# Kernel tuning notes

Measured on AMD Instinct MI355X. Metric: run time of the kernel, lower is better.

## Reference

```python
import jax, jax.numpy as jnp
import numpy as np

jax.config.update("jax_enable_x64", True)  # 64-bit hashes for collision-free WL signatures

N_NODES = 100_000
N_FEATURES = 64
N_EDGES = 6_400_000
NUM_ITERATIONS = 3
STEP = 1


def setup_inputs() -> dict:
    key = jax.random.key(0)
    kx, ke = jax.random.split(key)
    x = jax.random.normal(kx, (N_NODES, N_FEATURES), dtype=jnp.float32)  # one-hot-ish label scores
    edge_index = jax.random.randint(ke, (2, N_EDGES), 0, N_NODES, dtype=jnp.int64)
    return {"x": x, "edge_index": edge_index}


def _splitmix64(z):
    # High-quality 64-bit mixer (uint64, wraps mod 2^64).
    z = z + jnp.uint64(0x9E3779B97F4A7C15)
    z = (z ^ (z >> jnp.uint64(30))) * jnp.uint64(0xBF58476D1CE4E5B9)
    z = (z ^ (z >> jnp.uint64(27))) * jnp.uint64(0x94D049BB133111EB)
    return z ^ (z >> jnp.uint64(31))


def _wl_conv(colors, src, dst, offset):
    """One WL refinement: hash (own color, multiset of neighbor colors), then
    relabel signatures by first-occurrence order (matches PyG WLConv's dict
    insertion order), continuing the global color counter `offset` (matches the
    persistent hashmap across iterations)."""
    n = colors.shape[0]
    h = _splitmix64(colors.astype(jnp.uint64) + jnp.uint64(1))
    # multiset of neighbor colors -> order-invariant sum of neighbor hashes
    nb_sum = jnp.zeros(n, dtype=jnp.uint64).at[dst].add(h[src])  # [N]
    sig = _splitmix64(h * jnp.uint64(0x100000001B3) + nb_sum)    # [N] signatures
    # first-occurrence relabeling (stable, deterministic)
    _, inv = jnp.unique(sig, size=n, fill_value=jnp.uint64(0), return_inverse=True)
    idx = jnp.arange(n, dtype=jnp.int64)
    first_idx = jax.ops.segment_min(idx, inv, num_segments=n)  # empty segments -> int64 max
    order = jnp.argsort(first_idx)                              # real uniques come first
    ranks = jnp.zeros(n, dtype=jnp.int64).at[order].set(idx)
    new_colors = offset + ranks[inv]
    num_new = jnp.sum(first_idx < n).astype(jnp.int64)
    return new_colors, offset + num_new


def reference(x, edge_index):
    src, dst = edge_index[0], edge_index[1]
    colors = jnp.argmax(x, axis=1).astype(jnp.int64)  # [N]
    feats = [colors]
    offset = jnp.int64(0)
    for _ in range(NUM_ITERATIONS):
        for _ in range(STEP):
            colors, offset = _wl_conv(colors, src, dst, offset)
        feats.append(colors)
    return jnp.stack(feats, axis=-1)  # [N, NUM_ITERATIONS+1], int64
```

## Files before the change

### kernel.cpp

```cpp
#include <hip/hip_runtime.h>

typedef unsigned long long u64;
typedef unsigned int u32;

#define TBL_BITS 18
#define TBL_SIZE (1u << TBL_BITS)
#define TBL_MASK (TBL_SIZE - 1u)
#define EMPTY_KEY 0xFFFFFFFFFFFFFFFFull

#define NB   196
#define NBLK 128
#define CNT_ENTRIES (NB * NBLK)

__device__ __forceinline__ u64 splitmix64(u64 z) {
    z = z + 0x9E3779B97F4A7C15ull;
    z = (z ^ (z >> 30)) * 0xBF58476D1CE4E5B9ull;
    z = (z ^ (z >> 27)) * 0x94D049BB133111EBull;
    return z ^ (z >> 31);
}


__global__ void argmax_kernel(const float* __restrict__ x, u64* __restrict__ h,
                              int* __restrict__ out, u32* __restrict__ offsets, int n) {
    if (blockIdx.x == 0 && threadIdx.x == 0) offsets[0] = 0u;
    int wave = (int)((blockIdx.x * (u32)blockDim.x + threadIdx.x) >> 6);
    int lane = threadIdx.x & 63;
    if (wave >= n) return;
    float v = x[(size_t)wave * 64 + lane];
    int idx = lane;
    #pragma unroll
    for (int off = 32; off >= 1; off >>= 1) {
        float ov = __shfl_xor(v, off);
        int   oi = __shfl_xor(idx, off);
        if (ov > v || (ov == v && oi < idx)) { v = ov; idx = oi; }
    }
    if (lane == 0) {
        h[wave] = splitmix64((u64)idx + 1ull);
        out[(size_t)wave * 4 + 0] = idx;
    }
}

__global__ void sig_kernel(const u64* __restrict__ h, const u64* __restrict__ nb,
                           u64* __restrict__ sig, u64* __restrict__ keys,
                           u32* __restrict__ vals, int n) {
    int i = blockIdx.x * blockDim.x + threadIdx.x;
    if (i >= n) return;
    u64 s = splitmix64(h[i] * 0x100000001B3ull + nb[i]);
    sig[i] = s;
    u32 slot = (u32)s & TBL_MASK;
    while (true) {
        u64 prev = atomicCAS(&keys[slot], (u64)EMPTY_KEY, s);
        if (prev == EMPTY_KEY || prev == s) break;
        slot = (slot + 1u) & TBL_MASK;
    }
    atomicMin(&vals[slot], (u32)i);
}


__global__ __launch_bounds__(1024) void count_part(const int* __restrict__ dst,
                                                   u32* __restrict__ cnt, int m) {
    __shared__ u32 hist[NB];
    int t = threadIdx.x, b = blockIdx.x;
    if (t < NB) hist[t] = 0u;
    __syncthreads();
    int per = (m + NBLK - 1) / NBLK;
    int lo = b * per, hi = lo + per; if (hi > m) hi = m;
    for (int e = lo + t; e < hi; e += 1024) atomicAdd(&hist[((u32)dst[e]) >> 9], 1u);
    __syncthreads();
    if (t < NB) cnt[t * NBLK + b] = hist[t];
}

__global__ __launch_bounds__(1024) void scan_flat(const u32* __restrict__ cnt,
                                                  u32* __restrict__ off) {
    __shared__ u32 A[1024], B[1024];
    int t = threadIdx.x;
    int chunk = (CNT_ENTRIES + 1023) / 1024;
    int lo = t * chunk, hi = lo + chunk;
    if (lo > CNT_ENTRIES) lo = CNT_ENTRIES;
    if (hi > CNT_ENTRIES) hi = CNT_ENTRIES;
    u32 s = 0;
    for (int i = lo; i < hi; ++i) s += cnt[i];
    A[t] = s; __syncthreads();
    u32 *cur = A, *nxt = B;
    for (int o = 1; o < 1024; o <<= 1) {
        u32 v = cur[t] + ((t >= o) ? cur[t - o] : 0u);
        nxt[t] = v; __syncthreads();
        u32* tmp = cur; cur = nxt; nxt = tmp;
    }
    u32 run = cur[t] - s;
    for (int i = lo; i < hi; ++i) { off[i] = run; run += cnt[i]; }
}

__global__ __launch_bounds__(1024) void scatter_part(const int* __restrict__ src,
                                                     const int* __restrict__ dst,
                                                     const u32* __restrict__ off,
                                                     u32* __restrict__ packed, int m) {
    __shared__ u32 pos[NB];
    int t = threadIdx.x, b = blockIdx.x;
    if (t < NB) pos[t] = off[t * NBLK + b];
    __syncthreads();
    int per = (m + NBLK - 1) / NBLK;
    int lo = b * per, hi = lo + per; if (hi > m) hi = m;
    for (int e = lo + t; e < hi; e += 1024) {
        u32 d = (u32)dst[e];
        u32 p = atomicAdd(&pos[d >> 9], 1u);
        packed[p] = ((u32)src[e] << 9) | (d & 511u);
    }
}

__global__ __launch_bounds__(1024) void nb_kernel(const u32* __restrict__ packed,
                                                  const u32* __restrict__ off,
                                                  const u64* __restrict__ h,
                                                  u64* __restrict__ nb,
                                                  u64* __restrict__ keys,
                                                  u32* __restrict__ vals, int n, int m) {
    int b = blockIdx.x, t = threadIdx.x;
    if (b >= NB) {
        int j = (b - NB) * 1024 + t;
        keys[j] = EMPTY_KEY; vals[j] = 0xFFFFFFFFu;
        return;
    }
    __shared__ u64 acc[512];
    if (t < 512) acc[t] = 0ull;
    __syncthreads();
    int lo = (int)off[b * NBLK];
    int hi = (b == NB - 1) ? m : (int)off[(b + 1) * NBLK];
    for (int e = lo + t; e < hi; e += 1024) {
        u32 p = packed[e];
        atomicAdd(&acc[p & 511u], h[p >> 9]);
    }
    __syncthreads();
    int base = b * 512;
    if (t < 512 && base + t < n) nb[base + t] = acc[t];
}

__global__ void count_rank(const u64* __restrict__ sig, const u64* __restrict__ keys,
                           const u32* __restrict__ vals, u32* __restrict__ f,
                           u32* __restrict__ lrank, u32* __restrict__ partials, int n) {
    int b = blockIdx.x, t = threadIdx.x;
    int i = b * 256 + t;
    u32 isf = 0, fi = 0;
    if (i < n) {
        u64 s = sig[i];
        u32 slot = (u32)s & TBL_MASK;
        while (keys[slot] != s) slot = (slot + 1u) & TBL_MASK;
        fi = vals[slot];
        f[i] = fi;
        isf = (fi == (u32)i) ? 1u : 0u;
    }
    __shared__ u32 wsum[4];
    u32 lane = t & 63, wv = (u32)t >> 6;
    int x = (int)isf;
    #pragma unroll
    for (int o = 1; o < 64; o <<= 1) {
        int y = __shfl_up(x, o);
        if (lane >= (u32)o) x += y;
    }
    if (lane == 63) wsum[wv] = (u32)x;
    __syncthreads();
    u32 woff = 0;
    for (u32 w = 0; w < wv; ++w) woff += wsum[w];
    if (i < n) lrank[i] = woff + (u32)x - isf;
    if (t == 255) partials[b] = woff + (u32)x;
}

__global__ void scan_partials(const u32* __restrict__ partials, u32* __restrict__ pp,
                              u32* __restrict__ offsets, int iter, int nblk) {
    __shared__ u32 A[512], B[512];
    int t = threadIdx.x;
    u32 v = (t < nblk) ? partials[t] : 0u;
    A[t] = v; __syncthreads();
    u32 *cur = A, *nxt = B;
    for (int o = 1; o < 512; o <<= 1) {
        u32 y = cur[t] + ((t >= o) ? cur[t - o] : 0u);
        nxt[t] = y; __syncthreads();
        u32* tmp = cur; cur = nxt; nxt = tmp;
    }
    if (t < nblk) pp[t] = cur[t] - v;
    if (t == 511) offsets[iter + 1] = offsets[iter] + cur[511];
}

__global__ void relabel_fast(const u32* __restrict__ f, const u32* __restrict__ lrank,
                             const u32* __restrict__ pp, const u32* __restrict__ offsets,
                             int iter, u64* __restrict__ h, int* __restrict__ out, int n) {
    int i = blockIdx.x * 256 + threadIdx.x;
    if (i >= n) return;
    u32 j = f[i];
    u32 c = offsets[iter] + pp[j >> 8] + lrank[j];
    h[i] = splitmix64((u64)c + 1ull);
    out[(size_t)i * 4 + (iter + 1)] = (int)c;
}


__global__ void init_iter_kernel(u64* __restrict__ keys, u32* __restrict__ vals,
                                 u64* __restrict__ nb, int n) {
    int i = blockIdx.x * blockDim.x + threadIdx.x;
    if (i < (int)TBL_SIZE) { keys[i] = EMPTY_KEY; vals[i] = 0xFFFFFFFFu; }
    if (i < n) nb[i] = 0ull;
}

__global__ void edge_kernel(const int* __restrict__ src, const int* __restrict__ dst,
                            const u64* __restrict__ h, u64* __restrict__ nb, int m) {
    int stride = gridDim.x * blockDim.x;
    for (int e = blockIdx.x * blockDim.x + threadIdx.x; e < m; e += stride) {
        atomicAdd(&nb[(u32)dst[e]], h[(u32)src[e]]);
    }
}

extern "C" void kernel_launch(void* const* d_in, const int* in_sizes, int n_in,
                              void* d_out, int out_size, void* d_ws, size_t ws_size,
                              hipStream_t stream) {
    const float* x = (const float*)d_in[0];
    const int* ei = (const int*)d_in[1];
    int n = in_sizes[0] / 64;
    int m = in_sizes[1] / 2;
    const int* src = ei;
    const int* dst = ei + m;
    int* out = (int*)d_out;

    const int NPB = (n + 255) / 256;

    auto align = [](size_t v) { return (v + 255) & ~(size_t)255; };
    size_t sz_packed = align((size_t)m * 4);
    size_t sz_cnt    = align((size_t)CNT_ENTRIES * 4);
    size_t sz_h      = align((size_t)n * 8);
    size_t sz_tblk   = align((size_t)TBL_SIZE * 8);
    size_t sz_tblv   = align((size_t)TBL_SIZE * 4);
    size_t sz_n4     = align((size_t)n * 4);
    size_t sz_small  = align((size_t)512 * 4);
    size_t need_fast = sz_packed + 2 * sz_cnt + 3 * sz_h + sz_tblk + sz_tblv
                     + 2 * sz_n4 + 2 * sz_small + 256;

    char* p = (char*)d_ws;
    if (ws_size >= need_fast) {
        u32* packed  = (u32*)p; p += sz_packed;
        u32* cnt     = (u32*)p; p += sz_cnt;
        u32* off     = (u32*)p; p += sz_cnt;
        u64* h       = (u64*)p; p += sz_h;
        u64* nb      = (u64*)p; p += sz_h;
        u64* sig     = (u64*)p; p += sz_h;
        u64* keys    = (u64*)p; p += sz_tblk;
        u32* vals    = (u32*)p; p += sz_tblv;
        u32* f       = (u32*)p; p += sz_n4;
        u32* lrank   = (u32*)p; p += sz_n4;
        u32* partials= (u32*)p; p += sz_small;
        u32* pp      = (u32*)p; p += sz_small;
        u32* offsets = (u32*)p;

        argmax_kernel<<<(n + 3) / 4, 256, 0, stream>>>(x, h, out, offsets, n);
        count_part  <<<NBLK, 1024, 0, stream>>>(dst, cnt, m);
        scan_flat   <<<1, 1024, 0, stream>>>(cnt, off);
        scatter_part<<<NBLK, 1024, 0, stream>>>(src, dst, off, packed, m);

        for (int it = 0; it < 3; ++it) {
            nb_kernel    <<<NB + 256, 1024, 0, stream>>>(packed, off, h, nb, keys, vals, n, m);
            sig_kernel   <<<NPB, 256, 0, stream>>>(h, nb, sig, keys, vals, n);
            count_rank   <<<NPB, 256, 0, stream>>>(sig, keys, vals, f, lrank, partials, n);
            scan_partials<<<1, 512, 0, stream>>>(partials, pp, offsets, it, NPB);
            relabel_fast <<<NPB, 256, 0, stream>>>(f, lrank, pp, offsets, it, h, out, n);
        }
    } else {
        u64* h       = (u64*)p; p += sz_h;
        u64* nb      = (u64*)p; p += sz_h;
        u64* sig     = (u64*)p; p += sz_h;
        u64* keys    = (u64*)p; p += sz_tblk;
        u32* vals    = (u32*)p; p += sz_tblv;
        u32* f       = (u32*)p; p += sz_n4;
        u32* lrank   = (u32*)p; p += sz_n4;
        u32* partials= (u32*)p; p += sz_small;
        u32* pp      = (u32*)p; p += sz_small;
        u32* offsets = (u32*)p;

        argmax_kernel<<<(n + 3) / 4, 256, 0, stream>>>(x, h, out, offsets, n);
        for (int it = 0; it < 3; ++it) {
            init_iter_kernel<<<(TBL_SIZE + 255) / 256, 256, 0, stream>>>(keys, vals, nb, n);
            edge_kernel  <<<4096, 256, 0, stream>>>(src, dst, h, nb, m);
            sig_kernel   <<<NPB, 256, 0, stream>>>(h, nb, sig, keys, vals, n);
            count_rank   <<<NPB, 256, 0, stream>>>(sig, keys, vals, f, lrank, partials, n);
            scan_partials<<<1, 512, 0, stream>>>(partials, pp, offsets, it, NPB);
            relabel_fast <<<NPB, 256, 0, stream>>>(f, lrank, pp, offsets, it, h, out, n);
        }
    }
}
```

Baseline: 308.1 us.

## Use finer destination buckets with vectorized partitioning and cached hash slots

The edge partition moves from 196 buckets of 512 nodes to 782 buckets of 128 nodes, using 256 partition blocks and int4/uint4 vectorized loads. A two-level scan with 64-aligned bucket bases replaces the single-thread-block flat scan. The neighbor-sum kernel now runs many more small blocks, each with a 128-entry shared accumulator, to raise parallelism and cut shared-memory atomic footprint per block. The signature kernel also stores the hash-table slot so count_rank skips the re-probe and no longer needs the sig array. In exchange, the fast path only runs when the edge count is a multiple of 4 and the bucket count fits in 1024.

```diff
diff --git a/kernel.cpp b/kernel.cpp
--- a/kernel.cpp
+++ b/kernel.cpp
@@ -8,9 +8,10 @@
 #define TBL_MASK (TBL_SIZE - 1u)
 #define EMPTY_KEY 0xFFFFFFFFFFFFFFFFull
 
-#define NB   196
-#define NBLK 128
-#define CNT_ENTRIES (NB * NBLK)
+#define BK_BITS 7
+#define BK_SZ   128
+#define MAXNB   1024
+#define NBLK    256
 
 __device__ __forceinline__ u64 splitmix64(u64 z) {
     z = z + 0x9E3779B97F4A7C15ull;
@@ -18,7 +19,6 @@
     z = (z ^ (z >> 27)) * 0x94D049BB133111EBull;
     return z ^ (z >> 31);
 }
-
 
 __global__ void argmax_kernel(const float* __restrict__ x, u64* __restrict__ h,
                               int* __restrict__ out, u32* __restrict__ offsets, int n) {
@@ -40,13 +40,145 @@
     }
 }
 
+
+__global__ __launch_bounds__(1024) void count_part(const int* __restrict__ dst,
+                                                   u32* __restrict__ cnt, int m, int nbuck) {
+    __shared__ u32 hist[MAXNB];
+    int t = threadIdx.x, b = blockIdx.x;
+    for (int i = t; i < nbuck; i += 1024) hist[i] = 0u;
+    __syncthreads();
+    int mv = m >> 2;
+    int perv = (mv + NBLK - 1) / NBLK;
+    int lo = b * perv, hi = lo + perv; if (hi > mv) hi = mv;
+    const int4* d4 = (const int4*)dst;
+    for (int i = lo + t; i < hi; i += 1024) {
+        int4 v = d4[i];
+        atomicAdd(&hist[((u32)v.x) >> BK_BITS], 1u);
+        atomicAdd(&hist[((u32)v.y) >> BK_BITS], 1u);
+        atomicAdd(&hist[((u32)v.z) >> BK_BITS], 1u);
+        atomicAdd(&hist[((u32)v.w) >> BK_BITS], 1u);
+    }
+    if (b == 0 && t == 0)
+        for (int e = mv * 4; e < m; ++e) atomicAdd(&hist[((u32)dst[e]) >> BK_BITS], 1u);
+    __syncthreads();
+    for (int i = t; i < nbuck; i += 1024) cnt[i * NBLK + b] = hist[i];
+}
+
+__global__ void scan_bucket(u32* __restrict__ cnt, u32* __restrict__ total, int nbuck) {
+    int b = blockIdx.x, t = threadIdx.x;
+    u32 v = cnt[b * NBLK + t];
+    int lane = t & 63, w = t >> 6;
+    int x = (int)v;
+    #pragma unroll
+    for (int o = 1; o < 64; o <<= 1) {
+        int y = __shfl_up(x, o);
+        if (lane >= o) x += y;
+    }
+    __shared__ u32 ws[4];
+    if (lane == 63) ws[w] = (u32)x;
+    __syncthreads();
+    u32 woff = 0;
+    for (int ww = 0; ww < w; ++ww) woff += ws[ww];
+    u32 incl = woff + (u32)x;
+    cnt[b * NBLK + t] = incl - v;
+    if (t == 255) total[b] = incl;
+}
+
+__global__ __launch_bounds__(1024) void scan_bases(const u32* __restrict__ total,
+                                                   u32* __restrict__ bases, int nbuck) {
+    __shared__ u32 A[1024], B[1024];
+    int t = threadIdx.x;
+    u32 pt = (t < nbuck) ? ((total[t] + 63u) & ~63u) : 0u;
+    A[t] = pt; __syncthreads();
+    u32 *cur = A, *nxt = B;
+    for (int o = 1; o < 1024; o <<= 1) {
+        u32 y = cur[t] + ((t >= o) ? cur[t - o] : 0u);
+        nxt[t] = y; __syncthreads();
+        u32* tmp = cur; cur = nxt; nxt = tmp;
+    }
+    if (t < nbuck) bases[t] = cur[t] - pt;
+}
+
+__global__ __launch_bounds__(1024) void scatter_part(const int* __restrict__ src,
+                                                     const int* __restrict__ dst,
+                                                     const u32* __restrict__ cnt,
+                                                     const u32* __restrict__ bases,
+                                                     u32* __restrict__ packed, int m, int nbuck) {
+    __shared__ u32 pos[MAXNB];
+    int t = threadIdx.x, b = blockIdx.x;
+    for (int i = t; i < nbuck; i += 1024) pos[i] = bases[i] + cnt[i * NBLK + b];
+    __syncthreads();
+    int mv = m >> 2;
+    int perv = (mv + NBLK - 1) / NBLK;
+    int lo = b * perv, hi = lo + perv; if (hi > mv) hi = mv;
+    const int4* d4 = (const int4*)dst;
+    const int4* s4 = (const int4*)src;
+    for (int i = lo + t; i < hi; i += 1024) {
+        int4 dv = d4[i]; int4 sv = s4[i];
+        u32 d0 = (u32)dv.x, d1 = (u32)dv.y, d2 = (u32)dv.z, d3 = (u32)dv.w;
+        u32 p0 = atomicAdd(&pos[d0 >> BK_BITS], 1u);
+        packed[p0] = ((u32)sv.x << BK_BITS) | (d0 & (BK_SZ - 1u));
+        u32 p1 = atomicAdd(&pos[d1 >> BK_BITS], 1u);
+        packed[p1] = ((u32)sv.y << BK_BITS) | (d1 & (BK_SZ - 1u));
+        u32 p2 = atomicAdd(&pos[d2 >> BK_BITS], 1u);
+        packed[p2] = ((u32)sv.z << BK_BITS) | (d2 & (BK_SZ - 1u));
+        u32 p3 = atomicAdd(&pos[d3 >> BK_BITS], 1u);
+        packed[p3] = ((u32)sv.w << BK_BITS) | (d3 & (BK_SZ - 1u));
+    }
+    if (b == 0 && t == 0) {
+        for (int e = mv * 4; e < m; ++e) {
+            u32 d = (u32)dst[e];
+            u32 p = atomicAdd(&pos[d >> BK_BITS], 1u);
+            packed[p] = ((u32)src[e] << BK_BITS) | (d & (BK_SZ - 1u));
+        }
+    }
+}
+
+__global__ __launch_bounds__(256) void nb_kernel(const u32* __restrict__ packed,
+                                                 const u32* __restrict__ bases,
+                                                 const u32* __restrict__ total,
+                                                 const u64* __restrict__ h,
+                                                 u64* __restrict__ nb,
+                                                 u64* __restrict__ keys,
+                                                 u32* __restrict__ vals, int n, int nbuck) {
+    int b = blockIdx.x, t = threadIdx.x;
+    if (b >= nbuck) {
+        int base = (b - nbuck) * 1024;
+        for (int k = t; k < 1024; k += 256) { keys[base + k] = EMPTY_KEY; vals[base + k] = 0xFFFFFFFFu; }
+        return;
+    }
+    __shared__ u64 acc[BK_SZ];
+    if (t < BK_SZ) acc[t] = 0ull;
+    __syncthreads();
+    u32 lo = bases[b];
+    u32 len = total[b];
+    const uint4* p4 = (const uint4*)(packed + lo);
+    int len4 = (int)(len >> 2);
+    for (int i = t; i < len4; i += 256) {
+        uint4 v = p4[i];
+        atomicAdd(&acc[v.x & (BK_SZ - 1u)], h[v.x >> BK_BITS]);
+        atomicAdd(&acc[v.y & (BK_SZ - 1u)], h[v.y >> BK_BITS]);
+        atomicAdd(&acc[v.z & (BK_SZ - 1u)], h[v.z >> BK_BITS]);
+        atomicAdd(&acc[v.w & (BK_SZ - 1u)], h[v.w >> BK_BITS]);
+    }
+    for (int e = len4 * 4 + t; e < (int)len; e += 256) {
+        u32 v = packed[lo + e];
+        atomicAdd(&acc[v & (BK_SZ - 1u)], h[v >> BK_BITS]);
+    }
+    __syncthreads();
+    if (t < BK_SZ) {
+        int node = (b << BK_BITS) + t;
+        if (node < n) nb[node] = acc[t];
+    }
+}
+
+
 __global__ void sig_kernel(const u64* __restrict__ h, const u64* __restrict__ nb,
-                           u64* __restrict__ sig, u64* __restrict__ keys,
+                           u32* __restrict__ slotarr, u64* __restrict__ keys,
                            u32* __restrict__ vals, int n) {
     int i = blockIdx.x * blockDim.x + threadIdx.x;
     if (i >= n) return;
     u64 s = splitmix64(h[i] * 0x100000001B3ull + nb[i]);
-    sig[i] = s;
     u32 slot = (u32)s & TBL_MASK;
     while (true) {
         u64 prev = atomicCAS(&keys[slot], (u64)EMPTY_KEY, s);
@@ -54,97 +186,17 @@
         slot = (slot + 1u) & TBL_MASK;
     }
     atomicMin(&vals[slot], (u32)i);
-}
-
-
-__global__ __launch_bounds__(1024) void count_part(const int* __restrict__ dst,
-                                                   u32* __restrict__ cnt, int m) {
-    __shared__ u32 hist[NB];
-    int t = threadIdx.x, b = blockIdx.x;
-    if (t < NB) hist[t] = 0u;
-    __syncthreads();
-    int per = (m + NBLK - 1) / NBLK;
-    int lo = b * per, hi = lo + per; if (hi > m) hi = m;
-    for (int e = lo + t; e < hi; e += 1024) atomicAdd(&hist[((u32)dst[e]) >> 9], 1u);
-    __syncthreads();
-    if (t < NB) cnt[t * NBLK + b] = hist[t];
-}
-
-__global__ __launch_bounds__(1024) void scan_flat(const u32* __restrict__ cnt,
-                                                  u32* __restrict__ off) {
-    __shared__ u32 A[1024], B[1024];
-    int t = threadIdx.x;
-    int chunk = (CNT_ENTRIES + 1023) / 1024;
-    int lo = t * chunk, hi = lo + chunk;
-    if (lo > CNT_ENTRIES) lo = CNT_ENTRIES;
-    if (hi > CNT_ENTRIES) hi = CNT_ENTRIES;
-    u32 s = 0;
-    for (int i = lo; i < hi; ++i) s += cnt[i];
-    A[t] = s; __syncthreads();
-    u32 *cur = A, *nxt = B;
-    for (int o = 1; o < 1024; o <<= 1) {
-        u32 v = cur[t] + ((t >= o) ? cur[t - o] : 0u);
-        nxt[t] = v; __syncthreads();
-        u32* tmp = cur; cur = nxt; nxt = tmp;
-    }
-    u32 run = cur[t] - s;
-    for (int i = lo; i < hi; ++i) { off[i] = run; run += cnt[i]; }
-}
-
-__global__ __launch_bounds__(1024) void scatter_part(const int* __restrict__ src,
-                                                     const int* __restrict__ dst,
-                                                     const u32* __restrict__ off,
-                                                     u32* __restrict__ packed, int m) {
-    __shared__ u32 pos[NB];
-    int t = threadIdx.x, b = blockIdx.x;
-    if (t < NB) pos[t] = off[t * NBLK + b];
-    __syncthreads();
-    int per = (m + NBLK - 1) / NBLK;
-    int lo = b * per, hi = lo + per; if (hi > m) hi = m;
-    for (int e = lo + t; e < hi; e += 1024) {
-        u32 d = (u32)dst[e];
-        u32 p = atomicAdd(&pos[d >> 9], 1u);
-        packed[p] = ((u32)src[e] << 9) | (d & 511u);
-    }
-}
-
-__global__ __launch_bounds__(1024) void nb_kernel(const u32* __restrict__ packed,
-                                                  const u32* __restrict__ off,
-                                                  const u64* __restrict__ h,
-                                                  u64* __restrict__ nb,
-                                                  u64* __restrict__ keys,
-                                                  u32* __restrict__ vals, int n, int m) {
-    int b = blockIdx.x, t = threadIdx.x;
-    if (b >= NB) {
-        int j = (b - NB) * 1024 + t;
-        keys[j] = EMPTY_KEY; vals[j] = 0xFFFFFFFFu;
-        return;
-    }
-    __shared__ u64 acc[512];
-    if (t < 512) acc[t] = 0ull;
-    __syncthreads();
-    int lo = (int)off[b * NBLK];
-    int hi = (b == NB - 1) ? m : (int)off[(b + 1) * NBLK];
-    for (int e = lo + t; e < hi; e += 1024) {
-        u32 p = packed[e];
-        atomicAdd(&acc[p & 511u], h[p >> 9]);
-    }
-    __syncthreads();
-    int base = b * 512;
-    if (t < 512 && base + t < n) nb[base + t] = acc[t];
-}
-
-__global__ void count_rank(const u64* __restrict__ sig, const u64* __restrict__ keys,
-                           const u32* __restrict__ vals, u32* __restrict__ f,
-                           u32* __restrict__ lrank, u32* __restrict__ partials, int n) {
+    slotarr[i] = slot;
+}
+
+__global__ void count_rank(const u32* __restrict__ slotarr, const u32* __restrict__ vals,
+                           u32* __restrict__ f, u32* __restrict__ lrank,
+                           u32* __restrict__ partials, int n) {
     int b = blockIdx.x, t = threadIdx.x;
     int i = b * 256 + t;
     u32 isf = 0, fi = 0;
     if (i < n) {
-        u64 s = sig[i];
-        u32 slot = (u32)s & TBL_MASK;
-        while (keys[slot] != s) slot = (slot + 1u) & TBL_MASK;
-        fi = vals[slot];
+        fi = vals[slotarr[i]];
         f[i] = fi;
         isf = (fi == (u32)i) ? 1u : 0u;
     }
@@ -219,28 +271,32 @@
     int* out = (int*)d_out;
 
     const int NPB = (n + 255) / 256;
+    const int nbuck = (n + BK_SZ - 1) >> BK_BITS;
 
     auto align = [](size_t v) { return (v + 255) & ~(size_t)255; };
-    size_t sz_packed = align((size_t)m * 4);
-    size_t sz_cnt    = align((size_t)CNT_ENTRIES * 4);
+    size_t sz_packed = align((size_t)m * 4 + (size_t)MAXNB * 64 * 4);
+    size_t sz_cnt    = align((size_t)MAXNB * NBLK * 4);
+    size_t sz_bt     = align((size_t)MAXNB * 4);
     size_t sz_h      = align((size_t)n * 8);
     size_t sz_tblk   = align((size_t)TBL_SIZE * 8);
     size_t sz_tblv   = align((size_t)TBL_SIZE * 4);
     size_t sz_n4     = align((size_t)n * 4);
     size_t sz_small  = align((size_t)512 * 4);
-    size_t need_fast = sz_packed + 2 * sz_cnt + 3 * sz_h + sz_tblk + sz_tblv
-                     + 2 * sz_n4 + 2 * sz_small + 256;
+    size_t need_fast = sz_packed + sz_cnt + 2 * sz_bt + 2 * sz_h + sz_tblk + sz_tblv
+                     + 3 * sz_n4 + 2 * sz_small + 256;
 
     char* p = (char*)d_ws;
-    if (ws_size >= need_fast) {
+    bool fast = (ws_size >= need_fast) && (nbuck <= MAXNB) && ((m & 3) == 0) && (NPB <= 512);
+    if (fast) {
         u32* packed  = (u32*)p; p += sz_packed;
         u32* cnt     = (u32*)p; p += sz_cnt;
-        u32* off     = (u32*)p; p += sz_cnt;
+        u32* total   = (u32*)p; p += sz_bt;
+        u32* bases   = (u32*)p; p += sz_bt;
         u64* h       = (u64*)p; p += sz_h;
         u64* nb      = (u64*)p; p += sz_h;
-        u64* sig     = (u64*)p; p += sz_h;
         u64* keys    = (u64*)p; p += sz_tblk;
         u32* vals    = (u32*)p; p += sz_tblv;
+        u32* slotarr = (u32*)p; p += sz_n4;
         u32* f       = (u32*)p; p += sz_n4;
         u32* lrank   = (u32*)p; p += sz_n4;
         u32* partials= (u32*)p; p += sz_small;
@@ -248,23 +304,24 @@
         u32* offsets = (u32*)p;
 
         argmax_kernel<<<(n + 3) / 4, 256, 0, stream>>>(x, h, out, offsets, n);
-        count_part  <<<NBLK, 1024, 0, stream>>>(dst, cnt, m);
-        scan_flat   <<<1, 1024, 0, stream>>>(cnt, off);
-        scatter_part<<<NBLK, 1024, 0, stream>>>(src, dst, off, packed, m);
+        count_part  <<<NBLK, 1024, 0, stream>>>(dst, cnt, m, nbuck);
+        scan_bucket <<<nbuck, 256, 0, stream>>>(cnt, total, nbuck);
+        scan_bases  <<<1, 1024, 0, stream>>>(total, bases, nbuck);
+        scatter_part<<<NBLK, 1024, 0, stream>>>(src, dst, cnt, bases, packed, m, nbuck);
 
         for (int it = 0; it < 3; ++it) {
-            nb_kernel    <<<NB + 256, 1024, 0, stream>>>(packed, off, h, nb, keys, vals, n, m);
-            sig_kernel   <<<NPB, 256, 0, stream>>>(h, nb, sig, keys, vals, n);
-            count_rank   <<<NPB, 256, 0, stream>>>(sig, keys, vals, f, lrank, partials, n);
+            nb_kernel    <<<nbuck + 256, 256, 0, stream>>>(packed, bases, total, h, nb, keys, vals, n, nbuck);
+            sig_kernel   <<<NPB, 256, 0, stream>>>(h, nb, slotarr, keys, vals, n);
+            count_rank   <<<NPB, 256, 0, stream>>>(slotarr, vals, f, lrank, partials, n);
             scan_partials<<<1, 512, 0, stream>>>(partials, pp, offsets, it, NPB);
             relabel_fast <<<NPB, 256, 0, stream>>>(f, lrank, pp, offsets, it, h, out, n);
         }
     } else {
         u64* h       = (u64*)p; p += sz_h;
         u64* nb      = (u64*)p; p += sz_h;
-        u64* sig     = (u64*)p; p += sz_h;
         u64* keys    = (u64*)p; p += sz_tblk;
         u32* vals    = (u32*)p; p += sz_tblv;
+        u32* slotarr = (u32*)p; p += sz_n4;
         u32* f       = (u32*)p; p += sz_n4;
         u32* lrank   = (u32*)p; p += sz_n4;
         u32* partials= (u32*)p; p += sz_small;
@@ -275,8 +332,8 @@
         for (int it = 0; it < 3; ++it) {
             init_iter_kernel<<<(TBL_SIZE + 255) / 256, 256, 0, stream>>>(keys, vals, nb, n);
             edge_kernel  <<<4096, 256, 0, stream>>>(src, dst, h, nb, m);
-            sig_kernel   <<<NPB, 256, 0, stream>>>(h, nb, sig, keys, vals, n);
-            count_rank   <<<NPB, 256, 0, stream>>>(sig, keys, vals, f, lrank, partials, n);
+            sig_kernel   <<<NPB, 256, 0, stream>>>(h, nb, slotarr, keys, vals, n);
+            count_rank   <<<NPB, 256, 0, stream>>>(slotarr, vals, f, lrank, partials, n);
             scan_partials<<<1, 512, 0, stream>>>(partials, pp, offsets, it, NPB);
             relabel_fast <<<NPB, 256, 0, stream>>>(f, lrank, pp, offsets, it, h, out, n);
         }
```

Result: faster. 256.6 us (-16.7%).
